# Performance work log

Measured on AMD Instinct MI355X. Metric: run time of the kernel, lower is better.

## Reference

```python
import jax, jax.numpy as jnp
import numpy as np

VOCAB = 32000      # embedding vocab
EMBED = 300        # nn.Embedding embedding_dim
HID = 256          # sequence_size // 2 per direction (sequence_size=512)
N_COLS = 4096      # number of columns (split-delimited segments)
SEG_LEN = 8        # 7 description words + 1 SPLIT token per column
SPLIT_IDX = 0
T = N_COLS * SEG_LEN


def setup_inputs() -> dict:
    key = jax.random.key(0)
    ks = jax.random.split(key, 10)
    # tokens in [1, VOCAB), with SPLIT_IDX at the end of every SEG_LEN block
    seq = jax.random.randint(ks[0], (T,), 1, VOCAB)
    seq = seq.at[SEG_LEN - 1::SEG_LEN].set(SPLIT_IDX)
    s = 1.0 / np.sqrt(HID)  # torch LSTM default init range

    def u(k, shape):
        return jax.random.uniform(k, shape, jnp.float32, -s, s)

    return {
        "emb_table": jax.random.normal(ks[1], (VOCAB, EMBED), jnp.float32),
        "w_ih_f": u(ks[2], (4 * HID, EMBED)),
        "w_hh_f": u(ks[3], (4 * HID, HID)),
        "b_ih_f": u(ks[4], (4 * HID,)),
        "b_hh_f": u(ks[5], (4 * HID,)),
        "w_ih_b": u(ks[6], (4 * HID, EMBED)),
        "w_hh_b": u(ks[7], (4 * HID, HID)),
        "b_ih_b": u(ks[8], (4 * HID,)),
        "b_hh_b": u(ks[9], (4 * HID,)),
        "seq_s": seq,
    }


def _run_dir(xg, mask, w_hh, reverse):
    """Masked LSTM over time. xg: [L, N, 4H] precomputed input gates (+bias),
    mask: [L, N] validity per original time index. Returns final hidden [N, H]."""
    if reverse:
        xg = xg[::-1]
        mask = mask[::-1]
    N = xg.shape[1]

    def step(carry, inp):
        h, c = carry
        g, m = inp
        gates = g + h @ w_hh.T                       # [N, 4H]
        i, f, gg, o = jnp.split(gates, 4, axis=-1)   # torch gate order i,f,g,o
        c_new = jax.nn.sigmoid(f) * c + jax.nn.sigmoid(i) * jnp.tanh(gg)
        h_new = jax.nn.sigmoid(o) * jnp.tanh(c_new)
        m = m[:, None]
        return (jnp.where(m, h_new, h), jnp.where(m, c_new, c)), None

    init = (jnp.zeros((N, HID), xg.dtype), jnp.zeros((N, HID), xg.dtype))
    (h, _), _ = jax.lax.scan(step, init, (xg, mask))
    return h


def reference(emb_table, w_ih_f, w_hh_f, b_ih_f, b_hh_f,
              w_ih_b, w_hh_b, b_ih_b, b_hh_b, seq_s):
    col = jnp.arange(N_COLS)
    # torch code: ends = nonzero(split); begins = roll(ends,1); begins[0] = 0
    # => segment i>0 starts AT the previous split token (len SEG_LEN);
    #    segment 0 is [0, SEG_LEN-1) (len SEG_LEN-1).
    begins = jnp.where(col == 0, 0, col * SEG_LEN - 1)
    lengths = jnp.where(col == 0, SEG_LEN - 1, SEG_LEN)
    idx = jnp.clip(begins[:, None] + jnp.arange(SEG_LEN)[None, :], 0, T - 1)  # [N, L]
    mask = jnp.arange(SEG_LEN)[None, :] < lengths[:, None]                    # [N, L]

    segs = emb_table[seq_s][idx]        # [N, L, E] embedded ragged segments
    x = segs.transpose(1, 0, 2)          # [L, N, E]
    m = mask.T                           # [L, N]

    xg_f = jnp.einsum('lne,ge->lng', x, w_ih_f) + b_ih_f + b_hh_f
    xg_b = jnp.einsum('lne,ge->lng', x, w_ih_b) + b_ih_b + b_hh_b
    h_f = _run_dir(xg_f, m, w_hh_f, reverse=False)   # forward final hidden
    h_b = _run_dir(xg_b, m, w_hh_b, reverse=True)    # backward final hidden (t=0)
    # torch final_hidden.view(-1) per column == concat(fwd, bwd)
    return jnp.concatenate([h_f, h_b], axis=-1)      # [N_COLS, 2*HID]
```

## Files before the change

kernel.cpp:

```cpp
#include <hip/hip_runtime.h>

typedef unsigned int uint;
typedef unsigned short ushort;
typedef __attribute__((ext_vector_type(8))) short short8;
typedef __attribute__((ext_vector_type(4))) float f32x4;
typedef __attribute__((ext_vector_type(4))) uint uint4w;

#define T_LEN 32768
#define EMB 300
#define HID 256
#define NCOLS 4096

__device__ __forceinline__ ushort f2bf(float f) {
  uint u = __float_as_uint(f);
  return (ushort)((u + 0x7fffu + ((u >> 16) & 1u)) >> 16);
}
__device__ __forceinline__ float bf2f(ushort u) {
  return __uint_as_float(((uint)u) << 16);
}
__device__ __forceinline__ float sigm(float x) { return 1.f / (1.f + __expf(-x)); }
__device__ __forceinline__ float tanh_(float x) { return 2.f / (1.f + __expf(-2.f * x)) - 1.f; }

__device__ __forceinline__ void gload_lds16(const void* g, void* l) {
  __builtin_amdgcn_global_load_lds((const __attribute__((address_space(1))) void*)g,
                                   (__attribute__((address_space(3))) void*)l, 16, 0, 0);
}

__global__ void prep_kernel(const float* __restrict__ emb,
                            const float* __restrict__ wihf, const float* __restrict__ whhf,
                            const float* __restrict__ bihf, const float* __restrict__ bhhf,
                            const float* __restrict__ wihb, const float* __restrict__ whhb,
                            const float* __restrict__ bihb, const float* __restrict__ bhhb,
                            const int* __restrict__ seq,
                            ushort* __restrict__ X, ushort* __restrict__ Wih,
                            ushort* __restrict__ Whh, float* __restrict__ bias) {
  const int NX = T_LEN * 40;
  const int NWIH = 2048 * 40;
  const int NWHH = 2048 * 32;
  const int NB = 2048;
  const int total = NX + NWIH + NWHH + NB;
  for (int t = blockIdx.x * blockDim.x + threadIdx.x; t < total; t += gridDim.x * blockDim.x) {
    if (t < NX) {
      int r = t / 40, k8 = t % 40, k = k8 * 8;
      int col = r >> 3, j = r & 7;
      int tok = (col == 0) ? j : (col * 8 - 1 + j);
      const float* src = emb + (long)seq[tok] * EMB + k;
      alignas(16) ushort tmp[8];
#pragma unroll
      for (int i = 0; i < 8; ++i) tmp[i] = (k + i < EMB) ? f2bf(src[i]) : (ushort)0;
      *(uint4w*)(X + (long)r * 320 + k) = *(const uint4w*)tmp;
    } else if (t < NX + NWIH) {
      int t2 = t - NX;
      int n = t2 / 40, k8 = t2 % 40, k = k8 * 8;
      const float* src = ((n < 1024) ? wihf : wihb) + (long)(n & 1023) * EMB + k;
      alignas(16) ushort tmp[8];
#pragma unroll
      for (int i = 0; i < 8; ++i) tmp[i] = (k + i < EMB) ? f2bf(src[i]) : (ushort)0;
      *(uint4w*)(Wih + (long)n * 320 + k) = *(const uint4w*)tmp;
    } else if (t < NX + NWIH + NWHH) {
      int t3 = t - NX - NWIH;
      int n = t3 / 32, k8 = t3 % 32, k = k8 * 8;
      const float* src = ((n < 1024) ? whhf : whhb) + (long)(n & 1023) * HID + k;
      alignas(16) ushort tmp[8];
#pragma unroll
      for (int i = 0; i < 8; ++i) tmp[i] = f2bf(src[i]);
      *(uint4w*)(Whh + (long)n * 256 + k) = *(const uint4w*)tmp;
    } else {
      int n = t - NX - NWIH - NWHH;
      bias[n] = (n < 1024) ? (bihf[n] + bhhf[n]) : (bihb[n - 1024] + bhhb[n - 1024]);
    }
  }
}

__global__ void gemm_xg_kernel(const ushort* __restrict__ X, const ushort* __restrict__ Wih,
                               const float* __restrict__ bias, ushort* __restrict__ xg) {
  __shared__ ushort a_lds[2][128 * 32];
  const int tid = threadIdx.x;
  const int lane = tid & 63, w = tid >> 6;
  const int wr = w >> 1, wc = w & 1;
  const int qrow = lane >> 4, ln = lane & 15;
  const int m0 = blockIdx.x * 128, n0 = blockIdx.y * 128;

  auto stage = [&](int buf, int kt) {
#pragma unroll
    for (int q = 0; q < 2; ++q) {
      int byteoff = w * 2048 + q * 1024 + lane * 16;
      int row = byteoff >> 6, koff = byteoff & 63;
      const char* src = (const char*)X + (long)(m0 + row) * 640 + kt * 64 + koff;
      void* dst = (char*)&a_lds[buf][0] + w * 2048 + q * 1024;
      gload_lds16(src, dst);
    }
  };

  const f32x4 fzero = {0.f, 0.f, 0.f, 0.f};
  f32x4 acc[4][4];
#pragma unroll
  for (int i = 0; i < 4; ++i)
#pragma unroll
    for (int jj = 0; jj < 4; ++jj) acc[i][jj] = fzero;

  stage(0, 0);
#pragma unroll 1
  for (int kt = 0; kt < 10; ++kt) {
    __syncthreads();
    if (kt < 9) stage((kt + 1) & 1, kt + 1);
    const int buf = kt & 1;
    short8 a[4], b[4];
#pragma unroll
    for (int rt = 0; rt < 4; ++rt)
      a[rt] = *(const short8*)&a_lds[buf][(wr * 64 + rt * 16 + ln) * 32 + qrow * 8];
#pragma unroll
    for (int nt = 0; nt < 4; ++nt)
      b[nt] = *(const short8*)(Wih + (long)(n0 + wc * 64 + nt * 16 + ln) * 320 + kt * 32 + qrow * 8);
#pragma unroll
    for (int rt = 0; rt < 4; ++rt)
#pragma unroll
      for (int nt = 0; nt < 4; ++nt)
        acc[rt][nt] = __builtin_amdgcn_mfma_f32_16x16x32_bf16(a[rt], b[nt], acc[rt][nt], 0, 0, 0);
  }

  ushort* sbuf = &a_lds[0][0];
  float bv[4];
#pragma unroll
  for (int nt = 0; nt < 4; ++nt) bv[nt] = bias[n0 + wc * 64 + nt * 16 + ln];
#pragma unroll
  for (int R = 0; R < 4; ++R) {
    __syncthreads();
#pragma unroll
    for (int nt = 0; nt < 4; ++nt)
#pragma unroll
      for (int r = 0; r < 4; ++r)
        sbuf[(wr * 16 + qrow * 4 + r) * 128 + wc * 64 + nt * 16 + ln] = f2bf(acc[R][nt][r] + bv[nt]);
    __syncthreads();
#pragma unroll
    for (int p = 0; p < 2; ++p) {
      int row = p * 16 + (tid >> 4);
      int c0 = (tid & 15) * 8;
      uint4w v = *(uint4w*)&sbuf[row * 128 + c0];
      *(uint4w*)&xg[(long)(m0 + (row >> 4) * 64 + R * 16 + (row & 15)) * 2048 + n0 + c0] = v;
    }
  }
}

__global__ __launch_bounds__(512, 2) void lstm_kernel(const ushort* __restrict__ xg,
                                                      const ushort* __restrict__ Whh,
                                                      float* __restrict__ out) {
  __shared__ ushort h_lds[32][264];
  __shared__ ushort xg_lds[2][32][1024];
  const int tid = threadIdx.x;
  const int lane = tid & 63, w = tid >> 6;
  const int qrow = lane >> 4, ln = lane & 15;
  const int bid = blockIdx.x;
  const int d = bid >> 7, cg = bid & 127;

  short8 bw[8][4][2];
#pragma unroll
  for (int ks = 0; ks < 8; ++ks)
#pragma unroll
    for (int g = 0; g < 4; ++g)
#pragma unroll
      for (int q = 0; q < 2; ++q)
        bw[ks][g][q] = *(const short8*)(Whh +
            (long)(d * 1024 + g * 256 + w * 32 + q * 16 + ln) * 256 + ks * 32 + qrow * 8);

  float c_st[2][2][4], h_st[2][2][4];
#pragma unroll
  for (int rt = 0; rt < 2; ++rt)
#pragma unroll
    for (int q = 0; q < 2; ++q)
#pragma unroll
      for (int r = 0; r < 4; ++r) { c_st[rt][q][r] = 0.f; h_st[rt][q][r] = 0.f; }

  auto stage = [&](int buf, int j) {
#pragma unroll
    for (int q = 0; q < 8; ++q) {
      int byteoff = w * 8192 + q * 1024 + lane * 16;
      int cloc = byteoff >> 11, noff = byteoff & 2047;
      const char* src = (const char*)xg + (long)((cg * 32 + cloc) * 8 + j) * 4096 + d * 2048 + noff;
      void* dst = (char*)&xg_lds[0][0][0] + buf * 65536 + w * 8192 + q * 1024;
      gload_lds16(src, dst);
    }
  };

  const f32x4 fzero = {0.f, 0.f, 0.f, 0.f};

  stage(0, d ? 7 : 0);

#pragma unroll 1
  for (int it = 0; it < 8; ++it) {
    __syncthreads();
    if (it < 7) stage((it + 1) & 1, d ? (6 - it) : (it + 1));
    const int buf = it & 1;

    f32x4 acc[4][2][2];
#pragma unroll
    for (int g = 0; g < 4; ++g)
#pragma unroll
      for (int q = 0; q < 2; ++q)
#pragma unroll
        for (int rt = 0; rt < 2; ++rt) acc[g][q][rt] = fzero;

    if (it > 0) {
#pragma unroll
      for (int ks = 0; ks < 8; ++ks) {
        short8 a0 = *(const short8*)&h_lds[ln][ks * 32 + qrow * 8];
        short8 a1 = *(const short8*)&h_lds[16 + ln][ks * 32 + qrow * 8];
#pragma unroll
        for (int g = 0; g < 4; ++g)
#pragma unroll
          for (int q = 0; q < 2; ++q) {
            acc[g][q][0] = __builtin_amdgcn_mfma_f32_16x16x32_bf16(a0, bw[ks][g][q], acc[g][q][0], 0, 0, 0);
            acc[g][q][1] = __builtin_amdgcn_mfma_f32_16x16x32_bf16(a1, bw[ks][g][q], acc[g][q][1], 0, 0, 0);
          }
      }
    }
    asm volatile("s_waitcnt lgkmcnt(0)" ::: "memory");
    __builtin_amdgcn_s_barrier();

    const bool mstep = d ? (it == 0) : (it == 7);
#pragma unroll
    for (int rt = 0; rt < 2; ++rt)
#pragma unroll
      for (int q = 0; q < 2; ++q)
#pragma unroll
        for (int r = 0; r < 4; ++r) {
          int cc = rt * 16 + qrow * 4 + r;
          int hid = w * 32 + q * 16 + ln;
          float pi = acc[0][q][rt][r] + bf2f(xg_lds[buf][cc][hid]);
          float pf = acc[1][q][rt][r] + bf2f(xg_lds[buf][cc][256 + hid]);
          float pg = acc[2][q][rt][r] + bf2f(xg_lds[buf][cc][512 + hid]);
          float po = acc[3][q][rt][r] + bf2f(xg_lds[buf][cc][768 + hid]);
          float cn = sigm(pf) * c_st[rt][q][r] + sigm(pi) * tanh_(pg);
          float hn = sigm(po) * tanh_(cn);
          bool skip = mstep && (cg == 0) && (cc == 0);
          if (!skip) { c_st[rt][q][r] = cn; h_st[rt][q][r] = hn; }
          h_lds[cc][hid] = f2bf(h_st[rt][q][r]);
        }
  }

#pragma unroll
  for (int rt = 0; rt < 2; ++rt)
#pragma unroll
    for (int q = 0; q < 2; ++q)
#pragma unroll
      for (int r = 0; r < 4; ++r) {
        int cc = rt * 16 + qrow * 4 + r;
        int hid = w * 32 + q * 16 + ln;
        out[(long)(cg * 32 + cc) * 512 + d * 256 + hid] = h_st[rt][q][r];
      }
}

extern "C" void kernel_launch(void* const* d_in, const int* in_sizes, int n_in,
                              void* d_out, int out_size, void* d_ws, size_t ws_size,
                              hipStream_t stream) {
  const float* emb  = (const float*)d_in[0];
  const float* wihf = (const float*)d_in[1];
  const float* whhf = (const float*)d_in[2];
  const float* bihf = (const float*)d_in[3];
  const float* bhhf = (const float*)d_in[4];
  const float* wihb = (const float*)d_in[5];
  const float* whhb = (const float*)d_in[6];
  const float* bihb = (const float*)d_in[7];
  const float* bhhb = (const float*)d_in[8];
  const int*   seq  = (const int*)d_in[9];
  float* out = (float*)d_out;

  char* ws = (char*)d_ws;
  ushort* xg   = (ushort*)(ws);
  ushort* X    = (ushort*)(ws + 134217728);
  ushort* Wih  = (ushort*)(ws + 155189248);
  ushort* Whh  = (ushort*)(ws + 156499968);
  float*  bias = (float*)(ws + 157548544);

  prep_kernel<<<dim3(1024), dim3(256), 0, stream>>>(emb, wihf, whhf, bihf, bhhf,
                                                    wihb, whhb, bihb, bhhb, seq,
                                                    X, Wih, Whh, bias);
  gemm_xg_kernel<<<dim3(256, 16), dim3(256), 0, stream>>>(X, Wih, bias, xg);
  lstm_kernel<<<dim3(256), dim3(512), 0, stream>>>(xg, Whh, out);
}
```

Before: 274.8 us.

## Stream recurrent weights from global with double-buffered registers; pipeline Wih loads

In the LSTM kernel, the full W_hh slice (8x4x2 short8, 256 VGPRs) is no longer held in registers across time steps. It is re-read from global/L2 each step, with a two-stage register double buffer so loads overlap the MFMAs. In the input-projection GEMM, the K loop is unrolled by two and the B operand is prefetched one step ahead. This frees registers, which may allow better occupancy or less spilling, at the cost of repeated weight traffic from L2 on every recurrent step of the serial chain.

New measurement: 280.0 us. Within noise of the previous version (+1.9%).

```diff
diff --git a/kernel.cpp b/kernel.cpp
--- a/kernel.cpp
+++ b/kernel.cpp
@@ -92,6 +92,13 @@
     }
   };
 
+  const ushort* wb = Wih + (long)(n0 + wc * 64 + ln) * 320 + qrow * 8;
+  auto loadB = [&](short8 (&dst)[4], int kt) {
+#pragma unroll
+    for (int nt = 0; nt < 4; ++nt)
+      dst[nt] = *(const short8*)(wb + nt * 16 * 320 + kt * 32);
+  };
+
   const f32x4 fzero = {0.f, 0.f, 0.f, 0.f};
   f32x4 acc[4][4];
 #pragma unroll
@@ -99,24 +106,32 @@
 #pragma unroll
     for (int jj = 0; jj < 4; ++jj) acc[i][jj] = fzero;
 
-  stage(0, 0);
-#pragma unroll 1
-  for (int kt = 0; kt < 10; ++kt) {
-    __syncthreads();
-    if (kt < 9) stage((kt + 1) & 1, kt + 1);
-    const int buf = kt & 1;
-    short8 a[4], b[4];
+  auto gemmK = [&](short8 (&b)[4], int buf) {
+    short8 a[4];
 #pragma unroll
     for (int rt = 0; rt < 4; ++rt)
       a[rt] = *(const short8*)&a_lds[buf][(wr * 64 + rt * 16 + ln) * 32 + qrow * 8];
 #pragma unroll
-    for (int nt = 0; nt < 4; ++nt)
-      b[nt] = *(const short8*)(Wih + (long)(n0 + wc * 64 + nt * 16 + ln) * 320 + kt * 32 + qrow * 8);
-#pragma unroll
     for (int rt = 0; rt < 4; ++rt)
 #pragma unroll
       for (int nt = 0; nt < 4; ++nt)
         acc[rt][nt] = __builtin_amdgcn_mfma_f32_16x16x32_bf16(a[rt], b[nt], acc[rt][nt], 0, 0, 0);
+  };
+
+  short8 bA[4], bB[4];
+  stage(0, 0);
+  loadB(bA, 0);
+#pragma unroll 1
+  for (int kt2 = 0; kt2 < 5; ++kt2) {
+    const int kt = kt2 * 2;
+    __syncthreads();
+    if (kt < 9) stage(1, kt + 1);
+    loadB(bB, kt + 1);
+    gemmK(bA, 0);
+    __syncthreads();
+    if (kt + 2 < 10) stage(0, kt + 2);
+    if (kt2 < 4) loadB(bA, kt + 2);
+    gemmK(bB, 1);
   }
 
   ushort* sbuf = &a_lds[0][0];
@@ -153,15 +168,7 @@
   const int bid = blockIdx.x;
   const int d = bid >> 7, cg = bid & 127;
 
-  short8 bw[8][4][2];
-#pragma unroll
-  for (int ks = 0; ks < 8; ++ks)
-#pragma unroll
-    for (int g = 0; g < 4; ++g)
-#pragma unroll
-      for (int q = 0; q < 2; ++q)
-        bw[ks][g][q] = *(const short8*)(Whh +
-            (long)(d * 1024 + g * 256 + w * 32 + q * 16 + ln) * 256 + ks * 32 + qrow * 8);
+  const ushort* wbase = Whh + (long)(d * 1024 + w * 32 + ln) * 256 + qrow * 8;
 
   float c_st[2][2][4], h_st[2][2][4];
 #pragma unroll
@@ -201,18 +208,35 @@
         for (int rt = 0; rt < 2; ++rt) acc[g][q][rt] = fzero;
 
     if (it > 0) {
-#pragma unroll
-      for (int ks = 0; ks < 8; ++ks) {
+      auto loadB = [&](short8 (&dst)[4][2], int ks) {
+#pragma unroll
+        for (int g = 0; g < 4; ++g)
+#pragma unroll
+          for (int q = 0; q < 2; ++q)
+            dst[g][q] = *(const short8*)(wbase + g * 65536 + q * 4096 + ks * 32);
+      };
+      auto gemmK = [&](short8 (&b)[4][2], int ks) {
         short8 a0 = *(const short8*)&h_lds[ln][ks * 32 + qrow * 8];
         short8 a1 = *(const short8*)&h_lds[16 + ln][ks * 32 + qrow * 8];
 #pragma unroll
         for (int g = 0; g < 4; ++g)
 #pragma unroll
           for (int q = 0; q < 2; ++q) {
-            acc[g][q][0] = __builtin_amdgcn_mfma_f32_16x16x32_bf16(a0, bw[ks][g][q], acc[g][q][0], 0, 0, 0);
-            acc[g][q][1] = __builtin_amdgcn_mfma_f32_16x16x32_bf16(a1, bw[ks][g][q], acc[g][q][1], 0, 0, 0);
+            acc[g][q][0] = __builtin_amdgcn_mfma_f32_16x16x32_bf16(a0, b[g][q], acc[g][q][0], 0, 0, 0);
+            acc[g][q][1] = __builtin_amdgcn_mfma_f32_16x16x32_bf16(a1, b[g][q], acc[g][q][1], 0, 0, 0);
           }
-      }
+      };
+      short8 bA[4][2], bB[4][2];
+      loadB(bA, 0);
+      loadB(bB, 1);
+      gemmK(bA, 0); loadB(bA, 2);
+      gemmK(bB, 1); loadB(bB, 3);
+      gemmK(bA, 2); loadB(bA, 4);
+      gemmK(bB, 3); loadB(bB, 5);
+      gemmK(bA, 4); loadB(bA, 6);
+      gemmK(bB, 5); loadB(bB, 7);
+      gemmK(bA, 6);
+      gemmK(bB, 7);
     }
     asm volatile("s_waitcnt lgkmcnt(0)" ::: "memory");
     __builtin_amdgcn_s_barrier();
```
